# Kernel tuning notes

Measured on AMD Instinct MI355X. Metric: run time of the kernel, lower is better.

Reference implementation:

```python
import jax, jax.numpy as jnp
import numpy as np

B, N, M, D, H, K, V = 2, 2048, 2048, 1024, 16, 64, 64
MAX_WAVELENGTH = 10000
SCALE_FACTOR = 1.0


def rope(x, positions, max_wavelength, scale_factor):
    # x: [b, s, h, k]; positions: [b, s] int
    head_dim = x.shape[-1]
    fraction = 2.0 * jnp.arange(head_dim // 2, dtype=x.dtype) / head_dim
    timescale = jnp.asarray(max_wavelength, x.dtype) ** fraction            # [k/2]
    # scaled positions -> phase per (b, s, 1 head bcast, k/2)
    phase = (positions.astype(x.dtype) / scale_factor)[:, :, None, None] / timescale  # [b,s,1,k/2]
    sin, cos = jnp.sin(phase), jnp.cos(phase)
    x1, x2 = jnp.split(x, 2, axis=-1)
    return jnp.concatenate([x1 * cos - x2 * sin, x2 * cos + x1 * sin], axis=-1)


def setup_inputs() -> dict:
    key = jax.random.key(0)
    ks = jax.random.split(key, 8)
    scale = 1.0 / np.sqrt(D)  # keep logits numerically sane with random params
    inp = {
        "query": jax.random.normal(ks[0], (B, N, D), jnp.float32),
        "q_positions": jnp.broadcast_to(jnp.arange(N, dtype=jnp.int32), (B, N)),
        "key": jax.random.normal(ks[1], (B, M, D), jnp.float32),
        "k_positions": jnp.broadcast_to(jnp.arange(M, dtype=jnp.int32), (B, M)),
        "value": jax.random.normal(ks[2], (B, M, D), jnp.float32),
        "mask": jnp.ones((1, 1, N, M), dtype=bool),
        "P_q": jax.random.normal(ks[3], (H, D, K), jnp.float32) * scale,
        "P_k": jax.random.normal(ks[4], (H, D, K), jnp.float32) * scale,
        "P_v": jax.random.normal(ks[5], (H, D, V), jnp.float32) * scale,
        "P_o": jax.random.normal(ks[6], (H, D, V), jnp.float32) * scale,
    }
    return inp


def reference(query, q_positions, key, k_positions, value, mask, P_q, P_k, P_v, P_o):
    q = jnp.einsum('bnd,hdk->bnhk', query, P_q)
    k = jnp.einsum('bmd,hdk->bmhk', key, P_k)
    v = jnp.einsum('bmd,hdv->bmhv', value, P_v)
    q = rope(q, q_positions, MAX_WAVELENGTH, SCALE_FACTOR)
    k = rope(k, k_positions, MAX_WAVELENGTH, SCALE_FACTOR)
    logits = jnp.einsum('bnhk,bmhk->bhnm', q, k)
    if mask is not None:
        logits = jnp.where(mask, logits, -jnp.inf)
    weights = jax.nn.softmax(logits, axis=-1)
    o = jnp.einsum('bhnm,bmhv->bnhv', weights, v)
    return jnp.einsum('bnhv,hdv->bnd', o, P_o)
```

## Files before the change

kernel.cpp:

```cpp
#include <hip/hip_runtime.h>
#include <hip/hip_bf16.h>
#include <math.h>

#define B_ 2
#define N_ 2048
#define M_ 2048
#define D_ 1024
#define H_ 16


typedef _Float16 f16;
typedef f16  f16x2 __attribute__((ext_vector_type(2)));
typedef f16  f16x4 __attribute__((ext_vector_type(4)));
typedef f16  f16x8 __attribute__((ext_vector_type(8)));
typedef float f32x4  __attribute__((ext_vector_type(4)));
typedef float f32x16 __attribute__((ext_vector_type(16)));

#define MFMA16(a, b, c) __builtin_amdgcn_mfma_f32_16x16x32_f16((a), (b), (c), 0, 0, 0)
#define MFMA32(a, b, c) __builtin_amdgcn_mfma_f32_32x32x16_f16((a), (b), (c), 0, 0, 0)
#define LDST 72
#define EXP2(x) __builtin_amdgcn_exp2f(x)

#define GLOAD_LDS(g, l)                                             \
  __builtin_amdgcn_global_load_lds(                                 \
      (const __attribute__((address_space(1))) void*)(g),           \
      (__attribute__((address_space(3))) void*)(l), 16, 0, 0)

static __device__ __forceinline__ unsigned int pk2(float a, float b) {
  auto h = __builtin_amdgcn_cvt_pkrtz(a, b);
  return __builtin_bit_cast(unsigned int, h);
}
static __device__ __forceinline__ float max3f(float a, float b, float c) {
  return fmaxf(fmaxf(a, b), c);
}

__global__ __launch_bounds__(256) void prep_all(
    const float* __restrict__ Pq, const float* __restrict__ Pk,
    const float* __restrict__ Pv, const float* __restrict__ Po,
    const int* __restrict__ qpos, const int* __restrict__ kpos,
    const float* __restrict__ Aq, const float* __restrict__ Ak,
    const float* __restrict__ Av,
    f16* __restrict__ Ptq, f16* __restrict__ Ptk, f16* __restrict__ Ptv,
    f16* __restrict__ Wo, float2* __restrict__ tabq, float2* __restrict__ tabk,
    f16* __restrict__ A16q, f16* __restrict__ A16k, f16* __restrict__ A16v)
{
  __shared__ float Ts[64][65];
  const int z = blockIdx.y, x = blockIdx.x, tid = threadIdx.x;
  if (z < 3) {
    if (x >= 256) return;
    const float* P = (z == 0) ? Pq : (z == 1) ? Pk : Pv;
    f16* Pt = (z == 0) ? Ptq : (z == 1) ? Ptk : Ptv;
    const int d0 = (x & 15) * 64, h = x >> 4;
    #pragma unroll
    for (int it = 0; it < 4; ++it) {
      int fi = tid + 256 * it;
      int dr = fi >> 4, c4 = (fi & 15) << 2;
      float4 v = *(const float4*)(P + ((size_t)h * D_ + d0 + dr) * 64 + c4);
      Ts[dr][c4+0] = v.x; Ts[dr][c4+1] = v.y; Ts[dr][c4+2] = v.z; Ts[dr][c4+3] = v.w;
    }
    __syncthreads();
    const int c = tid >> 2, dp = (tid & 3) * 16;
    f16x8 w0, w1;
    #pragma unroll
    for (int i = 0; i < 8; ++i) { w0[i] = (f16)Ts[dp + i][c]; w1[i] = (f16)Ts[dp + 8 + i][c]; }
    f16* dst = Pt + ((size_t)h * 64 + c) * D_ + d0 + dp;
    *(f16x8*)dst = w0;
    *(f16x8*)(dst + 8) = w1;
  } else if (z == 3) {
    int e = (x * 256 + tid) * 4;
    if (e >= H_ * D_ * 64) return;
    int h = e >> 16, d = (e >> 6) & 1023, v = e & 63;
    float4 xx = *(const float4*)(Po + e);
    f16x4 w = {(f16)xx.x, (f16)xx.y, (f16)xx.z, (f16)xx.w};
    *(f16x4*)&Wo[(size_t)d * 1024 + h * 64 + v] = w;
  } else if (z < 6) {
    if (x >= 512) return;
    int idx = x * 256 + tid;
    int r = idx >> 5, c = idx & 31;
    const int* pos = (z == 4) ? qpos : kpos;
    float2* tab = (z == 4) ? tabq : tabk;
    float fpos = (float)pos[r];
    float inv_ts = exp2f(-(float)c * 0.4152410118609203f);
    float ph = fpos * inv_ts, sn, cs;
    sincosf(ph, &sn, &cs);
    tab[idx] = make_float2(cs, sn);
  } else {
    const float* s = (z == 6) ? Aq : (z == 7) ? Ak : Av;
    f16* d = (z == 6) ? A16q : (z == 7) ? A16k : A16v;
    size_t e = ((size_t)x * 256 + tid) * 16;
    #pragma unroll
    for (int half = 0; half < 2; ++half) {
      float4 v0 = *(const float4*)(s + e + half * 8);
      float4 v1 = *(const float4*)(s + e + half * 8 + 4);
      f16x8 w = {(f16)v0.x, (f16)v0.y, (f16)v0.z, (f16)v0.w,
                 (f16)v1.x, (f16)v1.y, (f16)v1.z, (f16)v1.w};
      *(f16x8*)(d + e + half * 8) = w;
    }
  }
}

__global__ __launch_bounds__(256) void gemm_fused(
    const f16* __restrict__ Aq, const f16* __restrict__ Ak,
    const f16* __restrict__ Av,
    const f16* __restrict__ Bq, const f16* __restrict__ Bk,
    const f16* __restrict__ Bv,
    const float2* __restrict__ tabq, const float2* __restrict__ tabk,
    f16* __restrict__ dq, f16* __restrict__ dk, f16* __restrict__ dv)
{
  __shared__ f16 As[128 * 64];
  __shared__ f16 Bs[128 * 64];
  const int tid = threadIdx.x, lane = tid & 63, wave = tid >> 6;
  const int quad = lane >> 4, l16 = lane & 15;
  const int lb = blockIdx.x + 8 * (int)blockIdx.y;
  const int xcd = lb & 7, t = lb >> 3;
  const int col0 = (t & 7) * 128;
  const int row0 = (xcd * 4 + (t >> 3)) * 128;
  const int op = blockIdx.z;
  const int wr = (wave >> 1) * 64, wc = (wave & 1) * 64;

  const f16* A  = (op == 0) ? Aq : (op == 1) ? Ak : Av;
  const f16* Bt = (op == 0) ? Bq : (op == 1) ? Bk : Bv;

  f32x4 acc[4][4] = {};
  const int srow = wave * 8 + (lane >> 3);
  const int scol = (lane & 7) * 8;

  for (int k0 = 0; k0 < 1024; k0 += 64) {
    __syncthreads();
    #pragma unroll
    for (int c = 0; c < 4; ++c) {
      GLOAD_LDS(A  + (size_t)(row0 + c * 32 + srow) * 1024 + k0 + scol,
                &As[c * 2048 + wave * 512 + lane * 8]);
      GLOAD_LDS(Bt + (size_t)(col0 + c * 32 + srow) * 1024 + k0 + scol,
                &Bs[c * 2048 + wave * 512 + lane * 8]);
    }
    __syncthreads();
    #pragma unroll
    for (int ks = 0; ks < 2; ++ks) {
      f16x8 af[4], bf[4];
      #pragma unroll
      for (int i = 0; i < 4; ++i)
        af[i] = *(const f16x8*)&As[(wr + i * 16 + l16) * 64 + ks * 32 + quad * 8];
      #pragma unroll
      for (int j = 0; j < 4; ++j)
        bf[j] = *(const f16x8*)&Bs[(wc + j * 16 + l16) * 64 + ks * 32 + quad * 8];
      #pragma unroll
      for (int i = 0; i < 4; ++i)
        #pragma unroll
        for (int j = 0; j < 4; ++j)
          acc[i][j] = MFMA16(af[i], bf[j], acc[i][j]);
    }
  }

  if (op == 2) {
    #pragma unroll
    for (int i = 0; i < 4; ++i) {
      int r = row0 + wr + i * 16 + quad * 4;
      int b = r >> 11, s = r & 2047;
      #pragma unroll
      for (int j = 0; j < 4; ++j) {
        int col = col0 + wc + j * 16 + l16;
        int h = col >> 6, v = col & 63;
        f16x4 w = {(f16)acc[i][j][0], (f16)acc[i][j][1],
                   (f16)acc[i][j][2], (f16)acc[i][j][3]};
        *(f16x4*)&dv[((size_t)(b * H_ + h) * 64 + v) * 2048 + s] = w;
      }
    }
  } else {
    const float2* tab = (op == 0) ? tabq : tabk;
    f16* oq = (op == 0) ? dq : dk;
    #pragma unroll
    for (int i = 0; i < 4; ++i) {
      #pragma unroll
      for (int reg = 0; reg < 4; ++reg) {
        int r = row0 + wr + i * 16 + quad * 4 + reg;
        int b = r >> 11, s = r & 2047;
        #pragma unroll
        for (int j = 0; j < 2; ++j) {
          int col = col0 + wc + j * 16 + l16;
          int h = col >> 6, c = col & 63;
          float2 cs = tab[r * 32 + c];
          float x1 = acc[i][j][reg], x2 = acc[i][j + 2][reg];
          size_t base = ((size_t)(b * H_ + h) * 2048 + s) * 64;
          oq[base + c]      = (f16)(x1 * cs.x - x2 * cs.y);
          oq[base + c + 32] = (f16)(x2 * cs.x + x1 * cs.y);
        }
      }
    }
  }
}

__global__ __launch_bounds__(512, 4) void flash7b(
    const f16* __restrict__ q, const f16* __restrict__ k,
    const f16* __restrict__ vt, f16* __restrict__ o)
{
  __shared__ __align__(16) char smem[4 * 64 * LDST * sizeof(f16)];

  const int tid = threadIdx.x, lane = tid & 63, wave = tid >> 6;
  const int g = wave >> 2, w4 = wave & 3;
  const int L = lane >> 5, nl = lane & 31;
  const int lin = blockIdx.x + 16 * (blockIdx.y + 16 * (int)blockIdx.z);
  const int xcd = lin & 7, t = lin >> 3;
  const int hb = xcd * 4 + (t >> 4);
  const int n0 = (t & 15) * 128;
  const int h = hb & 15, b = hb >> 4;

  f16* Ks  = (f16*)smem + (size_t)g * (64 * LDST);
  f16* Vts = (f16*)smem + (size_t)(2 + g) * (64 * LDST);

  const f16* qb = q  + (size_t)(b * H_ + h) * N_ * 64;
  const f16* kb = k  + (size_t)(b * H_ + h) * M_ * 64 + (size_t)g * 1024 * 64;
  const f16* vb = vt + (size_t)(b * H_ + h) * 64 * M_ + g * 1024;

  f16x8 qf[4];
  #pragma unroll
  for (int gg = 0; gg < 4; ++gg)
    qf[gg] = *(const f16x8*)(qb + (size_t)(n0 + w4 * 32 + nl) * 64 + gg * 16 + L * 8);

  f32x16 acc[2] = {};
  float mst = -INFINITY;
  float lst = 0.f;
  const float L2E = 1.4426950408889634f;

  const int gtid = tid & 255;
  const int srow = gtid >> 2, soff = (gtid & 3) * 16;

  f16x8 kp0 = *(const f16x8*)(kb + (size_t)srow * 64 + soff);
  f16x8 kp1 = *(const f16x8*)(kb + (size_t)srow * 64 + soff + 8);
  f16x8 vp0 = *(const f16x8*)(vb + (size_t)srow * M_ + soff);
  f16x8 vp1 = *(const f16x8*)(vb + (size_t)srow * M_ + soff + 8);

  for (int m0 = 0; m0 < 1024; m0 += 64) {
    __syncthreads();
    *(f16x8*)&Ks[srow * LDST + soff]      = kp0;
    *(f16x8*)&Ks[srow * LDST + soff + 8]  = kp1;
    *(f16x8*)&Vts[srow * LDST + soff]     = vp0;
    *(f16x8*)&Vts[srow * LDST + soff + 8] = vp1;
    __syncthreads();
    if (m0 + 64 < 1024) {
      kp0 = *(const f16x8*)(kb + (size_t)(m0 + 64 + srow) * 64 + soff);
      kp1 = *(const f16x8*)(kb + (size_t)(m0 + 64 + srow) * 64 + soff + 8);
      vp0 = *(const f16x8*)(vb + (size_t)srow * M_ + m0 + 64 + soff);
      vp1 = *(const f16x8*)(vb + (size_t)srow * M_ + m0 + 64 + soff + 8);
    }

    f32x16 s[2] = {};
    __builtin_amdgcn_s_setprio(1);
    #pragma unroll
    for (int u = 0; u < 2; ++u)
      #pragma unroll
      for (int gg = 0; gg < 4; ++gg) {
        f16x8 af = *(const f16x8*)&Ks[(u * 32 + nl) * LDST + gg * 16 + L * 8];
        s[u] = MFMA32(af, qf[gg], s[u]);
      }
    __builtin_amdgcn_s_setprio(0);

    float a11[11];
    #pragma unroll
    for (int i = 0; i < 10; ++i) {
      int j = 3 * i;
      float x0 = (j < 16) ? s[0][j] : s[1][j - 16];
      float x1 = (j + 1 < 16) ? s[0][j + 1] : s[1][j - 15];
      float x2 = (j + 2 < 16) ? s[0][j + 2] : s[1][j - 14];
      a11[i] = max3f(x0, x1, x2);
    }
    a11[10] = fmaxf(s[1][14], s[1][15]);
    float b4_0 = max3f(a11[0], a11[1], a11[2]);
    float b4_1 = max3f(a11[3], a11[4], a11[5]);
    float b4_2 = max3f(a11[6], a11[7], a11[8]);
    float b4_3 = fmaxf(a11[9], a11[10]);
    float mx = fmaxf(fmaxf(b4_0, b4_1), fmaxf(b4_2, b4_3));
    mx = fmaxf(mx, __shfl_xor(mx, 32));
    float mx2 = mx * L2E;
    float m_new = fmaxf(mst, mx2);

    if (!__all(mx2 - mst <= 8.0f)) {
      float alpha = EXP2(mst - m_new);
      #pragma unroll
      for (int u = 0; u < 2; ++u)
        #pragma unroll
        for (int r = 0; r < 16; ++r) acc[u][r] *= alpha;
      lst *= alpha;
      mst = m_new;
    }

    #pragma unroll
    for (int u = 0; u < 2; ++u)
      #pragma unroll
      for (int r = 0; r < 16; ++r)
        s[u][r] = EXP2(s[u][r] * L2E - mst);

    unsigned int qw[2][4][2];
    #pragma unroll
    for (int u = 0; u < 2; ++u)
      #pragma unroll
      for (int rq = 0; rq < 4; ++rq) {
        qw[u][rq][0] = pk2(s[u][rq * 4 + 0], s[u][rq * 4 + 1]);
        qw[u][rq][1] = pk2(s[u][rq * 4 + 2], s[u][rq * 4 + 3]);
      }

#if __has_builtin(__builtin_amdgcn_fdot2)
    {
      const f16x2 one2 = {(f16)1.0f, (f16)1.0f};
      float sum = 0.f;
      #pragma unroll
      for (int u = 0; u < 2; ++u)
        #pragma unroll
        for (int rq = 0; rq < 4; ++rq)
          #pragma unroll
          for (int w = 0; w < 2; ++w)
            sum = __builtin_amdgcn_fdot2(
                __builtin_bit_cast(f16x2, qw[u][rq][w]), one2, sum, false);
      sum += __shfl_xor(sum, 32);
      lst += sum;
    }
#else
    {
      float ts[16];
      #pragma unroll
      for (int r = 0; r < 16; ++r) ts[r] = s[0][r] + s[1][r];
      #pragma unroll
      for (int st = 8; st >= 1; st >>= 1)
        #pragma unroll
        for (int r = 0; r < st; ++r) ts[r] += ts[r + st];
      float sum = ts[0];
      sum += __shfl_xor(sum, 32);
      lst += sum;
    }
#endif

    union PBu { unsigned int w[4]; f16x8 v; } pb[4];
    #pragma unroll
    for (int u = 0; u < 2; ++u)
      #pragma unroll
      for (int gg = 0; gg < 2; ++gg)
        #pragma unroll
        for (int w = 0; w < 2; ++w) {
          unsigned int a = qw[u][2 * gg][w], bb = qw[u][2 * gg + 1][w];
          asm volatile("v_permlane32_swap_b32 %0, %1" : "+v"(a), "+v"(bb));
          pb[2 * u + gg].w[w]     = a;
          pb[2 * u + gg].w[2 + w] = bb;
        }

    __builtin_amdgcn_s_setprio(1);
    #pragma unroll
    for (int u = 0; u < 2; ++u)
      #pragma unroll
      for (int gg = 0; gg < 4; ++gg) {
        f16x8 vf = *(const f16x8*)&Vts[(u * 32 + nl) * LDST + gg * 16 + L * 8];
        acc[u] = MFMA32(vf, pb[gg].v, acc[u]);
      }
    __builtin_amdgcn_s_setprio(0);
  }

  float* mrg = (float*)smem;
  const int mb = (w4 * 64 + lane) * 34;
  __syncthreads();
  if (g == 1) {
    #pragma unroll
    for (int r = 0; r < 16; ++r) { mrg[mb + r] = acc[0][r]; mrg[mb + 16 + r] = acc[1][r]; }
    mrg[mb + 32] = mst;
    mrg[mb + 33] = lst;
  }
  __syncthreads();
  if (g == 0) {
    float m1 = mrg[mb + 32], l1 = mrg[mb + 33];
    float Mm = fmaxf(mst, m1);
    float a0 = EXP2(mst - Mm), a1 = EXP2(m1 - Mm);
    float invl = 1.0f / (a0 * lst + a1 * l1);
    f16* ob = o + ((size_t)(b * N_ + n0 + w4 * 32 + nl) * 1024) + h * 64;
    #pragma unroll
    for (int u = 0; u < 2; ++u)
      #pragma unroll
      for (int rq = 0; rq < 4; ++rq) {
        f16x4 w;
        #pragma unroll
        for (int j = 0; j < 4; ++j)
          w[j] = (f16)((a0 * acc[u][rq * 4 + j] + a1 * mrg[mb + u * 16 + rq * 4 + j]) * invl);
        *(f16x4*)&ob[u * 32 + 8 * rq + 4 * L] = w;
      }
  }
}

__global__ __launch_bounds__(256) void gemm_out(
    const f16* __restrict__ A, const f16* __restrict__ Bt,
    float* __restrict__ out)
{
  __shared__ f16 As[128 * 64];
  __shared__ f16 Bs[64 * 64];
  const int tid = threadIdx.x, lane = tid & 63, wave = tid >> 6;
  const int quad = lane >> 4, l16 = lane & 15;
  const int lb = blockIdx.x + 16 * (int)blockIdx.y;
  const int xcd = lb & 7, t = lb >> 3;
  const int col0 = (t & 15) * 64;
  const int row0 = (xcd * 4 + (t >> 4)) * 128;
  const int wr = (wave >> 1) * 64, wc = (wave & 1) * 32;

  f32x4 acc[4][2] = {};
  const int srow = wave * 8 + (lane >> 3);
  const int scol = (lane & 7) * 8;

  for (int k0 = 0; k0 < 1024; k0 += 64) {
    __syncthreads();
    #pragma unroll
    for (int c = 0; c < 4; ++c)
      GLOAD_LDS(A + (size_t)(row0 + c * 32 + srow) * 1024 + k0 + scol,
                &As[c * 2048 + wave * 512 + lane * 8]);
    #pragma unroll
    for (int c = 0; c < 2; ++c)
      GLOAD_LDS(Bt + (size_t)(col0 + c * 32 + srow) * 1024 + k0 + scol,
                &Bs[c * 2048 + wave * 512 + lane * 8]);
    __syncthreads();
    #pragma unroll
    for (int ks = 0; ks < 2; ++ks) {
      f16x8 af[4], bf[2];
      #pragma unroll
      for (int i = 0; i < 4; ++i)
        af[i] = *(const f16x8*)&As[(wr + i * 16 + l16) * 64 + ks * 32 + quad * 8];
      #pragma unroll
      for (int j = 0; j < 2; ++j)
        bf[j] = *(const f16x8*)&Bs[(wc + j * 16 + l16) * 64 + ks * 32 + quad * 8];
      #pragma unroll
      for (int i = 0; i < 4; ++i)
        #pragma unroll
        for (int j = 0; j < 2; ++j)
          acc[i][j] = MFMA16(af[i], bf[j], acc[i][j]);
    }
  }

  #pragma unroll
  for (int i = 0; i < 4; ++i)
    #pragma unroll
    for (int j = 0; j < 2; ++j)
      #pragma unroll
      for (int reg = 0; reg < 4; ++reg)
        out[(size_t)(row0 + wr + i * 16 + quad * 4 + reg) * 1024 +
            col0 + wc + j * 16 + l16] = acc[i][j][reg];
}

extern "C" void kernel_launch(void* const* d_in, const int* in_sizes, int n_in,
                              void* d_out, int out_size, void* d_ws, size_t ws_size,
                              hipStream_t stream) {
  (void)in_sizes; (void)n_in; (void)out_size; (void)ws_size;
  const float* query = (const float*)d_in[0];
  const int*   qpos  = (const int*)d_in[1];
  const float* key   = (const float*)d_in[2];
  const int*   kpos  = (const int*)d_in[3];
  const float* value = (const float*)d_in[4];
  const float* Pq = (const float*)d_in[6];
  const float* Pk = (const float*)d_in[7];
  const float* Pv = (const float*)d_in[8];
  const float* Po = (const float*)d_in[9];
  float* out = (float*)d_out;

  const size_t pm = (size_t)1024 * 1024;
  const size_t em = (size_t)B_ * H_ * 2048 * 64;
  f16* Ptq = (f16*)d_ws;
  f16* Ptk = Ptq + pm;
  f16* Ptv = Ptk + pm;
  f16* Wo  = Ptv + pm;
  f16* q_ws  = Wo + pm;
  f16* k_ws  = q_ws + em;
  f16* vt_ws = k_ws + em;
  f16* o_ws  = vt_ws + em;
  float2* tabq = (float2*)(o_ws + em);
  float2* tabk = tabq + (size_t)4096 * 32;
  f16* a16q = (f16*)(tabk + (size_t)4096 * 32);
  f16* a16k = a16q + em;
  f16* a16v = a16k + em;

  dim3 blk(256);
  prep_all<<<dim3(1024, 9), blk, 0, stream>>>(
      Pq, Pk, Pv, Po, qpos, kpos, query, key, value,
      Ptq, Ptk, Ptv, Wo, tabq, tabk, a16q, a16k, a16v);

  gemm_fused<<<dim3(8, 32, 3), blk, 0, stream>>>(
      a16q, a16k, a16v, Ptq, Ptk, Ptv, tabq, tabk, q_ws, k_ws, vt_ws);

  flash7b<<<dim3(N_ / 128, H_, B_), dim3(512), 0, stream>>>(q_ws, k_ws, vt_ws, o_ws);

  gemm_out<<<dim3(16, 32), blk, 0, stream>>>(o_ws, Wo, out);
}
```

Measured before the change: 241.5 us.

## Double-buffer LDS with XOR swizzle in projection and output GEMMs

Both the fused QKV projection GEMM and the output projection GEMM move from a single LDS buffer to two, so the next K-tile's global-to-LDS loads are issued while the MFMAs run on the current tile. The LDS layout gets an XOR swizzle on 16-byte columns to cut bank conflicts on the fragment reads, and the MFMA block is wrapped in s_setprio. This doubles LDS use per block, which may lower occupancy.

```diff
diff --git a/kernel.cpp b/kernel.cpp
--- a/kernel.cpp
+++ b/kernel.cpp
@@ -107,8 +107,8 @@
     const float2* __restrict__ tabq, const float2* __restrict__ tabk,
     f16* __restrict__ dq, f16* __restrict__ dk, f16* __restrict__ dv)
 {
-  __shared__ f16 As[128 * 64];
-  __shared__ f16 Bs[128 * 64];
+  __shared__ f16 As[2][128 * 64];
+  __shared__ f16 Bs[2][128 * 64];
   const int tid = threadIdx.x, lane = tid & 63, wave = tid >> 6;
   const int quad = lane >> 4, l16 = lane & 15;
   const int lb = blockIdx.x + 8 * (int)blockIdx.y;
@@ -123,34 +123,52 @@
 
   f32x4 acc[4][4] = {};
   const int srow = wave * 8 + (lane >> 3);
-  const int scol = (lane & 7) * 8;
-
-  for (int k0 = 0; k0 < 1024; k0 += 64) {
-    __syncthreads();
-    #pragma unroll
-    for (int c = 0; c < 4; ++c) {
-      GLOAD_LDS(A  + (size_t)(row0 + c * 32 + srow) * 1024 + k0 + scol,
-                &As[c * 2048 + wave * 512 + lane * 8]);
-      GLOAD_LDS(Bt + (size_t)(col0 + c * 32 + srow) * 1024 + k0 + scol,
-                &Bs[c * 2048 + wave * 512 + lane * 8]);
-    }
-    __syncthreads();
-    #pragma unroll
-    for (int ks = 0; ks < 2; ++ks) {
-      f16x8 af[4], bf[4];
-      #pragma unroll
-      for (int i = 0; i < 4; ++i)
-        af[i] = *(const f16x8*)&As[(wr + i * 16 + l16) * 64 + ks * 32 + quad * 8];
-      #pragma unroll
-      for (int j = 0; j < 4; ++j)
-        bf[j] = *(const f16x8*)&Bs[(wc + j * 16 + l16) * 64 + ks * 32 + quad * 8];
-      #pragma unroll
-      for (int i = 0; i < 4; ++i)
-        #pragma unroll
-        for (int j = 0; j < 4; ++j)
-          acc[i][j] = MFMA16(af[i], bf[j], acc[i][j]);
-    }
-  }
+  const int scol = ((lane & 7) ^ ((lane >> 3) & 7)) * 8;
+  const int sdst = wave * 512 + lane * 8;
+  const int rx   = l16 & 7;
+
+#define STAGE_F(b, kk)                                                       \
+  _Pragma("unroll")                                                          \
+  for (int c = 0; c < 4; ++c) {                                              \
+    GLOAD_LDS(A  + (size_t)(row0 + c * 32 + srow) * 1024 + (kk) + scol,      \
+              &As[b][c * 2048 + sdst]);                                      \
+    GLOAD_LDS(Bt + (size_t)(col0 + c * 32 + srow) * 1024 + (kk) + scol,      \
+              &Bs[b][c * 2048 + sdst]);                                      \
+  }
+
+#define COMPUTE_F(b)                                                         \
+  _Pragma("unroll")                                                          \
+  for (int ks = 0; ks < 2; ++ks) {                                           \
+    f16x8 af[4], bf[4];                                                      \
+    _Pragma("unroll")                                                        \
+    for (int i = 0; i < 4; ++i)                                              \
+      af[i] = *(const f16x8*)&As[b][(wr + i * 16 + l16) * 64 +               \
+                                    ((ks * 4 + quad) ^ rx) * 8];             \
+    _Pragma("unroll")                                                        \
+    for (int j = 0; j < 4; ++j)                                              \
+      bf[j] = *(const f16x8*)&Bs[b][(wc + j * 16 + l16) * 64 +               \
+                                    ((ks * 4 + quad) ^ rx) * 8];             \
+    __builtin_amdgcn_s_setprio(1);                                           \
+    _Pragma("unroll")                                                        \
+    for (int i = 0; i < 4; ++i)                                              \
+      _Pragma("unroll")                                                      \
+      for (int j = 0; j < 4; ++j)                                            \
+        acc[i][j] = MFMA16(af[i], bf[j], acc[i][j]);                         \
+    __builtin_amdgcn_s_setprio(0);                                           \
+  }
+
+  STAGE_F(0, 0);
+  __syncthreads();
+  for (int k0 = 0; k0 < 1024; k0 += 128) {
+    STAGE_F(1, k0 + 64);
+    COMPUTE_F(0);
+    __syncthreads();
+    if (k0 + 128 < 1024) STAGE_F(0, k0 + 128);
+    COMPUTE_F(1);
+    __syncthreads();
+  }
+#undef STAGE_F
+#undef COMPUTE_F
 
   if (op == 2) {
     #pragma unroll
@@ -386,8 +404,8 @@
     const f16* __restrict__ A, const f16* __restrict__ Bt,
     float* __restrict__ out)
 {
-  __shared__ f16 As[128 * 64];
-  __shared__ f16 Bs[64 * 64];
+  __shared__ f16 As[2][128 * 64];
+  __shared__ f16 Bs[2][64 * 64];
   const int tid = threadIdx.x, lane = tid & 63, wave = tid >> 6;
   const int quad = lane >> 4, l16 = lane & 15;
   const int lb = blockIdx.x + 16 * (int)blockIdx.y;
@@ -398,35 +416,53 @@
 
   f32x4 acc[4][2] = {};
   const int srow = wave * 8 + (lane >> 3);
-  const int scol = (lane & 7) * 8;
-
-  for (int k0 = 0; k0 < 1024; k0 += 64) {
-    __syncthreads();
-    #pragma unroll
-    for (int c = 0; c < 4; ++c)
-      GLOAD_LDS(A + (size_t)(row0 + c * 32 + srow) * 1024 + k0 + scol,
-                &As[c * 2048 + wave * 512 + lane * 8]);
-    #pragma unroll
-    for (int c = 0; c < 2; ++c)
-      GLOAD_LDS(Bt + (size_t)(col0 + c * 32 + srow) * 1024 + k0 + scol,
-                &Bs[c * 2048 + wave * 512 + lane * 8]);
-    __syncthreads();
-    #pragma unroll
-    for (int ks = 0; ks < 2; ++ks) {
-      f16x8 af[4], bf[2];
-      #pragma unroll
-      for (int i = 0; i < 4; ++i)
-        af[i] = *(const f16x8*)&As[(wr + i * 16 + l16) * 64 + ks * 32 + quad * 8];
-      #pragma unroll
-      for (int j = 0; j < 2; ++j)
-        bf[j] = *(const f16x8*)&Bs[(wc + j * 16 + l16) * 64 + ks * 32 + quad * 8];
-      #pragma unroll
-      for (int i = 0; i < 4; ++i)
-        #pragma unroll
-        for (int j = 0; j < 2; ++j)
-          acc[i][j] = MFMA16(af[i], bf[j], acc[i][j]);
-    }
-  }
+  const int scol = ((lane & 7) ^ ((lane >> 3) & 7)) * 8;
+  const int sdst = wave * 512 + lane * 8;
+  const int rx   = l16 & 7;
+
+#define STAGE_O(b, kk)                                                       \
+  _Pragma("unroll")                                                          \
+  for (int c = 0; c < 4; ++c)                                                \
+    GLOAD_LDS(A + (size_t)(row0 + c * 32 + srow) * 1024 + (kk) + scol,       \
+              &As[b][c * 2048 + sdst]);                                      \
+  _Pragma("unroll")                                                          \
+  for (int c = 0; c < 2; ++c)                                                \
+    GLOAD_LDS(Bt + (size_t)(col0 + c * 32 + srow) * 1024 + (kk) + scol,      \
+              &Bs[b][c * 2048 + sdst]);
+
+#define COMPUTE_O(b)                                                         \
+  _Pragma("unroll")                                                          \
+  for (int ks = 0; ks < 2; ++ks) {                                           \
+    f16x8 af[4], bf[2];                                                      \
+    _Pragma("unroll")                                                        \
+    for (int i = 0; i < 4; ++i)                                              \
+      af[i] = *(const f16x8*)&As[b][(wr + i * 16 + l16) * 64 +               \
+                                    ((ks * 4 + quad) ^ rx) * 8];             \
+    _Pragma("unroll")                                                        \
+    for (int j = 0; j < 2; ++j)                                              \
+      bf[j] = *(const f16x8*)&Bs[b][(wc + j * 16 + l16) * 64 +               \
+                                    ((ks * 4 + quad) ^ rx) * 8];             \
+    __builtin_amdgcn_s_setprio(1);                                           \
+    _Pragma("unroll")                                                        \
+    for (int i = 0; i < 4; ++i)                                              \
+      _Pragma("unroll")                                                      \
+      for (int j = 0; j < 2; ++j)                                            \
+        acc[i][j] = MFMA16(af[i], bf[j], acc[i][j]);                         \
+    __builtin_amdgcn_s_setprio(0);                                           \
+  }
+
+  STAGE_O(0, 0);
+  __syncthreads();
+  for (int k0 = 0; k0 < 1024; k0 += 128) {
+    STAGE_O(1, k0 + 64);
+    COMPUTE_O(0);
+    __syncthreads();
+    if (k0 + 128 < 1024) STAGE_O(0, k0 + 128);
+    COMPUTE_O(1);
+    __syncthreads();
+  }
+#undef STAGE_O
+#undef COMPUTE_O
 
   #pragma unroll
   for (int i = 0; i < 4; ++i)
```

Result: faster. 225.5 us (-6.6%).
